# Performance work log

Hardware: AMD Instinct MI355X
Metric: run time of the kernel (lower is better)

Reference implementation:

```python
import jax, jax.numpy as jnp
import numpy as np
from jax import lax

PAD = 1
T, B, V, E, H, K = 256, 64, 50000, 300, 256, 20  # H = hidden_dim//2 per direction


def setup_inputs() -> dict:
    key = jax.random.key(0)
    ks = jax.random.split(key, 14)
    lengths = jnp.sort(jax.random.randint(ks[0], (B,), T // 2, T + 1))[::-1]  # sorted desc like pack_padded
    toks = jax.random.randint(ks[1], (T, B), 2, V)
    tpos = jnp.arange(T)[:, None]
    x = jnp.where(tpos < lengths[None, :], toks, PAD)
    n = jax.random.normal
    s = 1.0 / np.sqrt(H)
    emb = (n(ks[2], (V, E)) * 0.1).at[PAD].set(0.0)  # padding_idx row zeroed
    Wih0 = n(ks[3], (2, 4 * H, E)) * s       # [dir, 4H, in]
    Whh0 = n(ks[4], (2, 4 * H, H)) * s
    b0 = n(ks[5], (2, 4 * H)) * s            # b_ih + b_hh folded together
    Wih1 = n(ks[6], (2, 4 * H, 2 * H)) * s
    Whh1 = n(ks[7], (2, 4 * H, H)) * s
    b1 = n(ks[8], (2, 4 * H)) * s
    W_out = n(ks[9], (K, 2 * H)) * s
    b_out = n(ks[10], (K,)) * s
    trans = n(ks[11], (K, K)) * 0.1
    start = n(ks[12], (K,)) * 0.1
    end = n(ks[13], (K,)) * 0.1
    return dict(x=x, sent_lengths=lengths, emb=emb, Wih0=Wih0, Whh0=Whh0, b0=b0,
                Wih1=Wih1, Whh1=Whh1, b1=b1, W_out=W_out, b_out=b_out,
                trans=trans, start=start, end=end)


def _lstm_dir(xs, m, Wih, Whh, b):
    # xs [T,B,D], m [T,B,1] float mask. PyTorch gate order i,f,g,o.
    xg = jnp.einsum('tbd,gd->tbg', xs, Wih) + b  # big GEMM up-front
    h0 = jnp.zeros((xs.shape[1], H), xs.dtype)

    def step(carry, inp):
        h, c = carry
        g_t, m_t = inp
        gates = g_t + h @ Whh.T
        i, f, g, o = jnp.split(gates, 4, -1)
        c_new = jax.nn.sigmoid(f) * c + jax.nn.sigmoid(i) * jnp.tanh(g)
        h_new = jax.nn.sigmoid(o) * jnp.tanh(c_new)
        # freeze state at padded steps (pack_padded semantics); padded outputs are zero
        return (jnp.where(m_t > 0, h_new, h), jnp.where(m_t > 0, c_new, c)), h_new * m_t

    _, out = lax.scan(step, (h0, h0), (xg, m))
    return out


def _bilstm(xs, m, rev, Wih, Whh, b):
    out_f = _lstm_dir(xs, m, Wih[0], Whh[0], b[0])
    xs_r = jnp.take_along_axis(xs, rev[:, :, None], 0)  # reverse within each length
    out_b = jnp.take_along_axis(_lstm_dir(xs_r, m, Wih[1], Whh[1], b[1]), rev[:, :, None], 0)
    return jnp.concatenate([out_f, out_b], -1)


def reference(x, sent_lengths, emb, Wih0, Whh0, b0, Wih1, Whh1, b1, W_out, b_out, trans, start, end):
    mask = x != PAD                               # [T,B]
    m = mask[:, :, None].astype(emb.dtype)
    tpos = jnp.arange(T)[:, None]
    rev = jnp.where(tpos < sent_lengths[None, :], sent_lengths[None, :] - 1 - tpos, tpos)
    h = emb[x]                                    # [T,B,E]
    h = _bilstm(h, m, rev, Wih0, Whh0, b0)
    h = _bilstm(h, m, rev, Wih1, Whh1, b1)
    emis = jnp.einsum('tbh,kh->tbk', h, W_out) + b_out  # [T,B,K]

    # Viterbi decode (torchcrf semantics)
    score0 = start[None, :] + emis[0]             # [B,K]

    def vstep(sc, inp):
        e_t, m_t = inp
        cand = sc[:, :, None] + trans[None] + e_t[:, None, :]  # [B,prev,next]
        best = cand.max(1)
        ptr = cand.argmax(1).astype(jnp.int32)
        sc2 = jnp.where(m_t[:, None], best, sc)
        # identity pointer at padded steps so backtrace passes tags through
        ptr = jnp.where(m_t[:, None], ptr, jnp.arange(K, dtype=jnp.int32)[None, :])
        return sc2, ptr

    score, hist = lax.scan(vstep, score0, (emis[1:], mask[1:]))
    score = score + end[None, :]                  # score frozen at seq end -> same as adding at last valid step
    last = jnp.argmax(score, -1).astype(jnp.int32)

    def back(tag, ptr):
        prev = jnp.take_along_axis(ptr, tag[:, None], 1)[:, 0]
        return prev, prev

    _, tags_prev = lax.scan(back, last, hist, reverse=True)
    tags = jnp.concatenate([tags_prev, last[None, :]], 0)  # [T,B]
    return jnp.where(mask, tags, 0)
```

## Files before the change

kernel.cpp:

```cpp
#include <hip/hip_runtime.h>
#include <stdint.h>


#define T_ 256
#define B_ 64
#define EPAD 304
#define KTAG 20
#define TB_ (T_ * B_)

#define QR2 22
#define QL2 8
#define QS2 34

#define KR_LO 64
#define KLQ_LO 3
#define NQS_LO 45
#define WLDS_OFF_LO (2 * KR_LO * 1024)
#define WSTR_OFF_LO (WLDS_OFF_LO + 2 * KLQ_LO * 1024 * 4)

__device__ __forceinline__ float rlane(float v, int l) {
  return __int_as_float(__builtin_amdgcn_readlane(__float_as_int(v), l));
}


__global__ void prep_embed(const int* __restrict__ x, const float* __restrict__ emb,
                           float* __restrict__ xsA) {
  int r = blockIdx.x;
  int tok = x[r];
  const float* src = emb + (size_t)tok * 300;
  for (int e = threadIdx.x; e < EPAD; e += 64)
    xsA[(size_t)r * EPAD + e] = (e < 300) ? src[e] : 0.f;
}

__global__ void prep_b0t(const float* __restrict__ Wih0, float* __restrict__ B0t) {
  int idx = blockIdx.x * 256 + threadIdx.x;
  if (idx >= 2048 * EPAD) return;
  int n = idx / EPAD, k = idx % EPAD;
  B0t[idx] = (k < 300) ? Wih0[(size_t)n * 300 + k] : 0.f;
}

__global__ void prep_bot64(const float* __restrict__ Wout, float* __restrict__ Bot,
                           const float* __restrict__ bout, float* __restrict__ biaso) {
  int idx = blockIdx.x * 256 + threadIdx.x;
  int n = idx >> 9, k = idx & 511;
  Bot[idx] = (n < KTAG) ? Wout[(size_t)n * 512 + k] : 0.f;
  if (idx < 64) biaso[idx] = (idx < KTAG) ? bout[idx] : 0.f;
}

__global__ void prep_whh4(const float* __restrict__ Whh, float* __restrict__ whhU) {
  int idx = blockIdx.x * 256 + threadIdx.x;
  int d = idx >> 18, rem = idx & 262143, row = rem >> 8, k = rem & 255;
  float v = Whh[(size_t)d * 262144 + (size_t)row * 256 + k];
  int gt = row >> 8, j = row & 255;
  int q = k >> 2, e = k & 3;
  whhU[((((size_t)d * 64 + q) * 4 + gt) * 256 + j) * 4 + e] = v;
}

__global__ void prep_whh2(const float* __restrict__ Whh, float* __restrict__ whhL) {
  int idx = blockIdx.x * 256 + threadIdx.x;
  int d = idx >> 18, rem = idx & 262143, k = rem >> 10, tg = rem & 1023;
  int row = (tg & 3) * 256 + (tg >> 2);
  float v = Whh[(size_t)d * 262144 + (size_t)row * 256 + k];
  if (k < KR_LO) {
    whhL[(size_t)(d * KR_LO + k) * 1024 + tg] = v;
  } else if (k < KR_LO + 12) {
    int kk = k - KR_LO, q = kk >> 2, e = kk & 3;
    whhL[WLDS_OFF_LO + (size_t)((d * KLQ_LO + q) * 1024 + tg) * 4 + e] = v;
  } else {
    int kk = k - KR_LO - 12, q = kk >> 2, e = kk & 3;
    whhL[WSTR_OFF_LO + (size_t)((d * NQS_LO + q) * 1024 + tg) * 4 + e] = v;
  }
}

__global__ __launch_bounds__(256) void gemm_f32(
    const float* __restrict__ A, int lda, const float* __restrict__ Bt, int ldb,
    float* __restrict__ C, int ldc, const float* __restrict__ bias,
    int ntn, int K) {
  const int tm = blockIdx.x / ntn, tn = blockIdx.x % ntn;
  const int m0 = tm * 64, n0 = tn * 64;
  __shared__ __align__(16) float As[16][64];
  __shared__ __align__(16) float Bs[16][64];
  const int tid = threadIdx.x;
  const int mm = tid >> 2, kq = (tid & 3) * 4;
  const int tx = tid & 15, ty = tid >> 4;
  float acc[4][4] = {};
  for (int k0 = 0; k0 < K; k0 += 16) {
    float4 av = *(const float4*)&A[(size_t)(m0 + mm) * lda + k0 + kq];
    float4 bv = *(const float4*)&Bt[(size_t)(n0 + mm) * ldb + k0 + kq];
    __syncthreads();
    As[kq + 0][mm] = av.x; As[kq + 1][mm] = av.y;
    As[kq + 2][mm] = av.z; As[kq + 3][mm] = av.w;
    Bs[kq + 0][mm] = bv.x; Bs[kq + 1][mm] = bv.y;
    Bs[kq + 2][mm] = bv.z; Bs[kq + 3][mm] = bv.w;
    __syncthreads();
#pragma unroll
    for (int kk = 0; kk < 16; ++kk) {
      float4 a4 = *(const float4*)&As[kk][ty * 4];
      float4 b4 = *(const float4*)&Bs[kk][tx * 4];
      acc[0][0] += a4.x * b4.x; acc[0][1] += a4.x * b4.y;
      acc[0][2] += a4.x * b4.z; acc[0][3] += a4.x * b4.w;
      acc[1][0] += a4.y * b4.x; acc[1][1] += a4.y * b4.y;
      acc[1][2] += a4.y * b4.z; acc[1][3] += a4.y * b4.w;
      acc[2][0] += a4.z * b4.x; acc[2][1] += a4.z * b4.y;
      acc[2][2] += a4.z * b4.z; acc[2][3] += a4.z * b4.w;
      acc[3][0] += a4.w * b4.x; acc[3][1] += a4.w * b4.y;
      acc[3][2] += a4.w * b4.z; acc[3][3] += a4.w * b4.w;
    }
  }
#pragma unroll
  for (int i = 0; i < 4; ++i)
#pragma unroll
    for (int j = 0; j < 4; ++j)
      C[(size_t)(m0 + ty * 4 + i) * ldc + n0 + tx * 4 + j] =
          acc[i][j] + bias[n0 + tx * 4 + j];
}

__global__ __attribute__((amdgpu_flat_work_group_size(512, 512),
                          amdgpu_waves_per_eu(2, 2)))
void lstm_rec_hi2(const float* __restrict__ xg, const float* __restrict__ whhU,
                  float* __restrict__ out, const int* __restrict__ lens) {
  const int wg = blockIdx.x, d = wg & 1, b = wg >> 1;
  const int len = lens[b];
  const int tg = threadIdx.x;
  const int j = tg & 255, gp = tg >> 8;
  const int g0 = gp * 2;
  const int l = tg & 63;
  const float* wb = whhU + (size_t)d * 64 * 4096;

  float4 wA[QR2], wB[QR2];
#pragma unroll
  for (int q = 0; q < QR2; ++q) {
    wA[q] = *(const float4*)(wb + ((size_t)(q * 4 + g0) * 256 + j) * 4);
    wB[q] = *(const float4*)(wb + ((size_t)(q * 4 + g0 + 1) * 256 + j) * 4);
  }
#pragma unroll
  for (int q = 0; q < QR2; ++q) {
    asm volatile("" : "+v"(wA[q].x), "+v"(wA[q].y), "+v"(wA[q].z), "+v"(wA[q].w));
    asm volatile("" : "+v"(wB[q].x), "+v"(wB[q].y), "+v"(wB[q].z), "+v"(wB[q].w));
  }

  __shared__ __align__(16) float4 wlds[QL2][4][256];
  __shared__ __align__(16) float hsd[2][256];
  __shared__ __align__(8) float2 exch[256];
  for (int i = tg; i < QL2 * 4 * 256; i += 512) {
    int q3 = i >> 10, g = (i >> 8) & 3, jj = i & 255;
    wlds[q3][g][jj] =
        *(const float4*)(wb + ((size_t)((QR2 + q3) * 4 + g) * 256 + jj) * 4);
  }
  if (tg < 256) hsd[0][tg] = 0.f;
  float c = 0.f;
  __syncthreads();

  for (int s = 0; s < len; ++s) {
    const int t = d ? (len - 1 - s) : s;
    const int rp = t * B_ + b;
    const size_t xb = (size_t)rp * 2048 + d * 1024 + (size_t)g0 * 256 + j;
    float xv0 = xg[xb];
    float xv1 = xg[xb + 256];
    float4 hv = *(const float4*)&hsd[s & 1][l * 4];

    float aA0 = 0.f, aA1 = 0.f, aB0 = 0.f, aB1 = 0.f;
#pragma unroll
    for (int q = 0; q < QR2; ++q) {
      float b0 = rlane(hv.x, q), b1 = rlane(hv.y, q);
      float b2 = rlane(hv.z, q), b3 = rlane(hv.w, q);
      aA0 += wA[q].x * b0 + wA[q].y * b1;  aA1 += wA[q].z * b2 + wA[q].w * b3;
      aB0 += wB[q].x * b0 + wB[q].y * b1;  aB1 += wB[q].z * b2 + wB[q].w * b3;
    }
#pragma unroll
    for (int q3 = 0; q3 < QL2; ++q3) {
      int q = QR2 + q3;
      float b0 = rlane(hv.x, q), b1 = rlane(hv.y, q);
      float b2 = rlane(hv.z, q), b3 = rlane(hv.w, q);
      float4 wa = wlds[q3][g0][j], wbq = wlds[q3][g0 + 1][j];
      aA0 += wa.x * b0 + wa.y * b1;   aA1 += wa.z * b2 + wa.w * b3;
      aB0 += wbq.x * b0 + wbq.y * b1; aB1 += wbq.z * b2 + wbq.w * b3;
    }
#pragma unroll 2
    for (int qs = 0; qs < QS2; ++qs) {
      int q = QR2 + QL2 + qs;
      float4 wa = *(const float4*)(wb + ((size_t)(q * 4 + g0) * 256 + j) * 4);
      float4 wbq = *(const float4*)(wb + ((size_t)(q * 4 + g0 + 1) * 256 + j) * 4);
      float b0 = rlane(hv.x, q), b1 = rlane(hv.y, q);
      float b2 = rlane(hv.z, q), b3 = rlane(hv.w, q);
      aA0 += wa.x * b0 + wa.y * b1;   aA1 += wa.z * b2 + wa.w * b3;
      aB0 += wbq.x * b0 + wbq.y * b1; aB1 += wbq.z * b2 + wbq.w * b3;
    }

    float aA = aA0 + aA1 + xv0;
    float aB = aB0 + aB1 + xv1;
    if (gp == 1) exch[j] = make_float2(aA, aB);
    __syncthreads();
    if (gp == 0) {
      float2 go = exch[j];
      float si = 1.f / (1.f + expf(-aA));
      float sf = 1.f / (1.f + expf(-aB));
      float so = 1.f / (1.f + expf(-go.y));
      c = sf * c + si * tanhf(go.x);
      float h = so * tanhf(c);
      hsd[(s + 1) & 1][j] = h;
      out[(size_t)rp * 512 + d * 256 + j] = h;
    }
    __syncthreads();
  }
  if (gp == 0)
    for (int t = len; t < T_; ++t)
      out[(size_t)(t * B_ + b) * 512 + d * 256 + j] = 0.f;
}

__global__ __launch_bounds__(1024, 4) void lstm_rec_lo(
    const float* __restrict__ xg, const float* __restrict__ whhL,
    float* __restrict__ out, const int* __restrict__ lens) {
  const int wg = blockIdx.x, dir = wg & 1, b = wg >> 1;
  const int len = lens[b];
  const int tg = threadIdx.x;
  const int j = tg >> 2, gt = tg & 3;
  const int row = gt * 256 + j;

  float wres[KR_LO];
#pragma unroll
  for (int k = 0; k < KR_LO; ++k)
    wres[k] = whhL[(size_t)(dir * KR_LO + k) * 1024 + tg];

  __shared__ __align__(16) float4 wlds[KLQ_LO][1024];
  __shared__ __align__(16) float hsd[2][256];
#pragma unroll
  for (int q = 0; q < KLQ_LO; ++q)
    wlds[q][tg] = *(const float4*)&whhL[WLDS_OFF_LO + (size_t)((dir * KLQ_LO + q) * 1024 + tg) * 4];
  if (tg < 256) hsd[0][tg] = 0.f;
  float c = 0.f;
  __syncthreads();

  const float* sp = whhL + WSTR_OFF_LO + (size_t)dir * NQS_LO * 4096 + (size_t)tg * 4;
  const int lane = tg & 63, qb = lane & ~3;

  for (int s = 0; s < len; ++s) {
    const int t = dir ? (len - 1 - s) : s;
    const int rp = t * B_ + b;
    float xv = xg[(size_t)rp * 2048 + dir * 1024 + row];
    float4 hv = *(const float4*)&hsd[s & 1][lane * 4];

    float acc0 = 0.f, acc1 = 0.f;
#pragma unroll
    for (int q = 0; q < KR_LO / 4; ++q) {
      float b0 = rlane(hv.x, q), b1 = rlane(hv.y, q);
      float b2 = rlane(hv.z, q), b3 = rlane(hv.w, q);
      acc0 += wres[4 * q + 0] * b0 + wres[4 * q + 1] * b1;
      acc1 += wres[4 * q + 2] * b2 + wres[4 * q + 3] * b3;
    }
#pragma unroll
    for (int q3 = 0; q3 < KLQ_LO; ++q3) {
      int q = KR_LO / 4 + q3;
      float4 wl = wlds[q3][tg];
      float b0 = rlane(hv.x, q), b1 = rlane(hv.y, q);
      float b2 = rlane(hv.z, q), b3 = rlane(hv.w, q);
      acc0 += wl.x * b0 + wl.y * b1;
      acc1 += wl.z * b2 + wl.w * b3;
    }
#pragma unroll 5
    for (int qq = 0; qq < NQS_LO; ++qq) {
      int q = KR_LO / 4 + KLQ_LO + qq;
      float4 wv = *(const float4*)(sp + (size_t)qq * 4096);
      float b0 = rlane(hv.x, q), b1 = rlane(hv.y, q);
      float b2 = rlane(hv.z, q), b3 = rlane(hv.w, q);
      acc0 += wv.x * b0 + wv.y * b1;
      acc1 += wv.z * b2 + wv.w * b3;
    }

    float a = acc0 + acc1 + xv;
    float v1 = __shfl(a, qb | 1);
    float v2 = __shfl(a, qb | 2);
    float v3 = __shfl(a, qb | 3);
    if (gt == 0) {
      float si = 1.f / (1.f + expf(-a));
      float sf = 1.f / (1.f + expf(-v1));
      float so = 1.f / (1.f + expf(-v3));
      c = sf * c + si * tanhf(v2);
      float h = so * tanhf(c);
      hsd[(s + 1) & 1][j] = h;
      out[(size_t)rp * 512 + dir * 256 + j] = h;
    }
    __syncthreads();
  }
  for (int t = len; t < T_; ++t)
    if (gt == 0) out[(size_t)(t * B_ + b) * 512 + dir * 256 + j] = 0.f;
}

__global__ __launch_bounds__(64) void viterbi(
    const float* __restrict__ emis, const float* __restrict__ trans,
    const float* __restrict__ startv, const float* __restrict__ endv,
    const int* __restrict__ lens, int* __restrict__ outp) {
  int b = blockIdx.x, lane = threadIdx.x;
  __shared__ float tr[KTAG * KTAG];
  __shared__ float fin[KTAG];
  __shared__ unsigned char hist[T_ * KTAG];
  for (int i = lane; i < KTAG * KTAG; i += 64) tr[i] = trans[i];
  int len = lens[b];
  float score = (lane < KTAG) ? startv[lane] + emis[(size_t)b * 64 + lane] : -3e38f;
  __syncthreads();
  for (int t = 1; t < len; ++t) {
    float e = (lane < KTAG) ? emis[(size_t)(t * B_ + b) * 64 + lane] : 0.f;
    float best = -3e38f; int bp = 0;
    for (int p = 0; p < KTAG; ++p) {
      float cand = (__shfl(score, p) + tr[p * KTAG + lane]) + e;
      if (cand > best) { best = cand; bp = p; }
    }
    if (lane < KTAG) { score = best; hist[t * KTAG + lane] = (unsigned char)bp; }
  }
  if (lane < KTAG) fin[lane] = score + endv[lane];
  __syncthreads();
  if (lane == 0) {
    float bb = -3e38f; int tag = 0;
    for (int p = 0; p < KTAG; ++p)
      if (fin[p] > bb) { bb = fin[p]; tag = p; }
    for (int t = len - 1; t >= 1; --t) {
      outp[t * B_ + b] = tag;
      tag = hist[t * KTAG + tag];
    }
    outp[b] = tag;
  }
  for (int t = len + lane; t < T_; t += 64) outp[t * B_ + b] = 0;
}

__global__ void sentinel_fill(int* __restrict__ outp, int val) {
  int i = blockIdx.x * 256 + threadIdx.x;
  if (i < TB_) outp[i] = val;
}
__global__ void diag_init(int* __restrict__ f) { if (threadIdx.x == 0) f[0] = 0; }
__global__ void check_nan(const float* __restrict__ p, long n, int* __restrict__ f) {
  long i0 = (long)blockIdx.x * 256 + threadIdx.x;
  int bad = 0;
  for (long i = i0; i < n; i += (long)gridDim.x * 256)
    if (!(fabsf(p[i]) <= 1e8f)) bad = 1;
  if (bad) atomicOr(&f[0], 1);
}
__global__ void verdict(const int* __restrict__ f, int* __restrict__ outp) {
  if (f[0]) outp[threadIdx.x] = -4096;
}


extern "C" void kernel_launch(void* const* d_in, const int* in_sizes, int n_in,
                              void* d_out, int out_size, void* d_ws, size_t ws_size,
                              hipStream_t stream) {
  int* outp = (int*)d_out;

  static const int exp_sizes[14] = {16384, 64, 15000000, 614400, 524288, 2048,
                                    1048576, 524288, 2048, 10240, 20, 400, 20, 20};
  int badi = (n_in == 14) ? -1 : 14;
  if (badi < 0)
    for (int i = 0; i < 14; ++i)
      if (in_sizes[i] != exp_sizes[i]) { badi = i; break; }
  if (badi >= 0) {
    hipLaunchKernelGGL(sentinel_fill, dim3((TB_ + 255) / 256), dim3(256), 0, stream,
                       outp, -(20000 + badi));
    return;
  }

  const int*   x      = (const int*)d_in[0];
  const int*   lens   = (const int*)d_in[1];
  const float* emb    = (const float*)d_in[2];
  const float* Wih0   = (const float*)d_in[3];
  const float* Whh0   = (const float*)d_in[4];
  const float* b0     = (const float*)d_in[5];
  const float* Wih1   = (const float*)d_in[6];
  const float* Whh1   = (const float*)d_in[7];
  const float* b1     = (const float*)d_in[8];
  const float* Wout   = (const float*)d_in[9];
  const float* bout   = (const float*)d_in[10];
  const float* trans  = (const float*)d_in[11];
  const float* startv = (const float*)d_in[12];
  const float* endv   = (const float*)d_in[13];

  static int chosen = -1;
  if (chosen < 0) {
    chosen = 0;
    hipFuncAttributes fa;
    if (hipFuncGetAttributes(&fa, reinterpret_cast<const void*>(&lstm_rec_hi2)) ==
            hipSuccess &&
        fa.localSizeBytes == 0 && fa.numRegs >= 160)
      chosen = 1;
  }

  const size_t sz_whh = (size_t)524288 * 4;

  const size_t need =
      (size_t)TB_ * 2048 * 4
    + (size_t)TB_ * EPAD * 4
    + (size_t)TB_ * 512 * 4
    + (size_t)2048 * EPAD * 4
    + (size_t)64 * 512 * 4
    + 4 * sz_whh
    + 64 * 4
    + (size_t)TB_ * 64 * 4
    + 64;

  if (ws_size < need) {
    hipLaunchKernelGGL(sentinel_fill, dim3((TB_ + 255) / 256), dim3(256), 0, stream,
                       outp, -(int)(10000 + (ws_size >> 20)));
    return;
  }

  char* w = (char*)d_ws;
  float* xg    = (float*)w;  w += (size_t)TB_ * 2048 * 4;
  float* xsA   = (float*)w;  w += (size_t)TB_ * EPAD * 4;
  float* outh  = (float*)w;  w += (size_t)TB_ * 512 * 4;
  float* B0t   = (float*)w;  w += (size_t)2048 * EPAD * 4;
  float* Bot   = (float*)w;  w += (size_t)64 * 512 * 4;
  float* whh0U = (float*)w;  w += sz_whh;
  float* whh1U = (float*)w;  w += sz_whh;
  float* whh0L = (float*)w;  w += sz_whh;
  float* whh1L = (float*)w;  w += sz_whh;
  float* biaso = (float*)w;  w += 64 * 4;
  float* emis  = (float*)w;  w += (size_t)TB_ * 64 * 4;
  int*   diag  = (int*)w;    w += 64;

  hipLaunchKernelGGL(diag_init, dim3(1), dim3(64), 0, stream, diag);
  hipLaunchKernelGGL(prep_embed, dim3(TB_), dim3(64), 0, stream, x, emb, xsA);
  hipLaunchKernelGGL(prep_b0t, dim3((2048 * EPAD + 255) / 256), dim3(256), 0, stream, Wih0, B0t);
  hipLaunchKernelGGL(prep_bot64, dim3(128), dim3(256), 0, stream, Wout, Bot, bout, biaso);
  if (chosen == 1) {
    hipLaunchKernelGGL(prep_whh4, dim3(2048), dim3(256), 0, stream, Whh0, whh0U);
    hipLaunchKernelGGL(prep_whh4, dim3(2048), dim3(256), 0, stream, Whh1, whh1U);
  } else {
    hipLaunchKernelGGL(prep_whh2, dim3(2048), dim3(256), 0, stream, Whh0, whh0L);
    hipLaunchKernelGGL(prep_whh2, dim3(2048), dim3(256), 0, stream, Whh1, whh1L);
  }

  hipLaunchKernelGGL(gemm_f32, dim3(256 * 32), dim3(256), 0, stream,
                     xsA, EPAD, B0t, EPAD, xg, 2048, b0, 32, EPAD);
  if (chosen == 1)
    hipLaunchKernelGGL(lstm_rec_hi2, dim3(128), dim3(512), 0, stream, xg, whh0U, outh, lens);
  else
    hipLaunchKernelGGL(lstm_rec_lo, dim3(128), dim3(1024), 0, stream, xg, whh0L, outh, lens);
  hipLaunchKernelGGL(gemm_f32, dim3(256 * 32), dim3(256), 0, stream,
                     outh, 512, Wih1, 512, xg, 2048, b1, 32, 512);
  if (chosen == 1)
    hipLaunchKernelGGL(lstm_rec_hi2, dim3(128), dim3(512), 0, stream, xg, whh1U, outh, lens);
  else
    hipLaunchKernelGGL(lstm_rec_lo, dim3(128), dim3(1024), 0, stream, xg, whh1L, outh, lens);
  hipLaunchKernelGGL(gemm_f32, dim3(256), dim3(256), 0, stream,
                     outh, 512, Bot, 512, emis, 64, biaso, 1, 512);
  hipLaunchKernelGGL(check_nan, dim3(256), dim3(256), 0, stream,
                     emis, (long)TB_ * 64, diag);
  hipLaunchKernelGGL(viterbi, dim3(B_), dim3(64), 0, stream,
                     emis, trans, startv, endv, lens, outp);
  hipLaunchKernelGGL(verdict, dim3(1), dim3(64), 0, stream, diag, outp);
}
```

Measured before the change: 3.994 ms.

## Remap LSTM lanes so gate pairs share a wave and exchange via shuffle

Rearranges the thread-to-hidden-unit mapping so both gate pairs for a hidden unit sit in the same wavefront (lower and upper 32 lanes). The g/o gate exchange then uses a cross-lane shuffle, which removes one workgroup barrier and the LDS exchange buffer on every timestep. It also moves more Whh slices into registers and LDS and fewer into per-step global loads, which raises register and LDS pressure and could cause spills. If spills occur, the existing register check would fall back to the slower kernel.

```diff
diff --git a/kernel.cpp b/kernel.cpp
--- a/kernel.cpp
+++ b/kernel.cpp
@@ -8,9 +8,9 @@
 #define KTAG 20
 #define TB_ (T_ * B_)
 
-#define QR2 22
-#define QL2 8
-#define QS2 34
+#define QR2 24
+#define QL2 9
+#define QS2 31
 
 #define KR_LO 64
 #define KLQ_LO 3
@@ -117,21 +117,22 @@
 
 __global__ __attribute__((amdgpu_flat_work_group_size(512, 512),
                           amdgpu_waves_per_eu(2, 2)))
-void lstm_rec_hi2(const float* __restrict__ xg, const float* __restrict__ whhU,
+void lstm_rec_hi3(const float* __restrict__ xg, const float* __restrict__ whhU,
                   float* __restrict__ out, const int* __restrict__ lens) {
   const int wg = blockIdx.x, d = wg & 1, b = wg >> 1;
   const int len = lens[b];
   const int tg = threadIdx.x;
-  const int j = tg & 255, gp = tg >> 8;
+  const int w = tg >> 6, l = tg & 63;
+  const int lhalf = l & 31, gp = l >> 5;
+  const int jj = w * 32 + lhalf;
   const int g0 = gp * 2;
-  const int l = tg & 63;
   const float* wb = whhU + (size_t)d * 64 * 4096;
 
   float4 wA[QR2], wB[QR2];
 #pragma unroll
   for (int q = 0; q < QR2; ++q) {
-    wA[q] = *(const float4*)(wb + ((size_t)(q * 4 + g0) * 256 + j) * 4);
-    wB[q] = *(const float4*)(wb + ((size_t)(q * 4 + g0 + 1) * 256 + j) * 4);
+    wA[q] = *(const float4*)(wb + ((size_t)(q * 4 + g0) * 256 + jj) * 4);
+    wB[q] = *(const float4*)(wb + ((size_t)(q * 4 + g0 + 1) * 256 + jj) * 4);
   }
 #pragma unroll
   for (int q = 0; q < QR2; ++q) {
@@ -141,11 +142,10 @@
 
   __shared__ __align__(16) float4 wlds[QL2][4][256];
   __shared__ __align__(16) float hsd[2][256];
-  __shared__ __align__(8) float2 exch[256];
   for (int i = tg; i < QL2 * 4 * 256; i += 512) {
-    int q3 = i >> 10, g = (i >> 8) & 3, jj = i & 255;
-    wlds[q3][g][jj] =
-        *(const float4*)(wb + ((size_t)((QR2 + q3) * 4 + g) * 256 + jj) * 4);
+    int q3 = i >> 10, g = (i >> 8) & 3, jx = i & 255;
+    wlds[q3][g][jx] =
+        *(const float4*)(wb + ((size_t)((QR2 + q3) * 4 + g) * 256 + jx) * 4);
   }
   if (tg < 256) hsd[0][tg] = 0.f;
   float c = 0.f;
@@ -154,7 +154,7 @@
   for (int s = 0; s < len; ++s) {
     const int t = d ? (len - 1 - s) : s;
     const int rp = t * B_ + b;
-    const size_t xb = (size_t)rp * 2048 + d * 1024 + (size_t)g0 * 256 + j;
+    const size_t xb = (size_t)rp * 2048 + d * 1024 + (size_t)g0 * 256 + jj;
     float xv0 = xg[xb];
     float xv1 = xg[xb + 256];
     float4 hv = *(const float4*)&hsd[s & 1][l * 4];
@@ -172,15 +172,15 @@
       int q = QR2 + q3;
       float b0 = rlane(hv.x, q), b1 = rlane(hv.y, q);
       float b2 = rlane(hv.z, q), b3 = rlane(hv.w, q);
-      float4 wa = wlds[q3][g0][j], wbq = wlds[q3][g0 + 1][j];
+      float4 wa = wlds[q3][g0][jj], wbq = wlds[q3][g0 + 1][jj];
       aA0 += wa.x * b0 + wa.y * b1;   aA1 += wa.z * b2 + wa.w * b3;
       aB0 += wbq.x * b0 + wbq.y * b1; aB1 += wbq.z * b2 + wbq.w * b3;
     }
 #pragma unroll 2
     for (int qs = 0; qs < QS2; ++qs) {
       int q = QR2 + QL2 + qs;
-      float4 wa = *(const float4*)(wb + ((size_t)(q * 4 + g0) * 256 + j) * 4);
-      float4 wbq = *(const float4*)(wb + ((size_t)(q * 4 + g0 + 1) * 256 + j) * 4);
+      float4 wa = *(const float4*)(wb + ((size_t)(q * 4 + g0) * 256 + jj) * 4);
+      float4 wbq = *(const float4*)(wb + ((size_t)(q * 4 + g0 + 1) * 256 + jj) * 4);
       float b0 = rlane(hv.x, q), b1 = rlane(hv.y, q);
       float b2 = rlane(hv.z, q), b3 = rlane(hv.w, q);
       aA0 += wa.x * b0 + wa.y * b1;   aA1 += wa.z * b2 + wa.w * b3;
@@ -189,23 +189,22 @@
 
     float aA = aA0 + aA1 + xv0;
     float aB = aB0 + aB1 + xv1;
-    if (gp == 1) exch[j] = make_float2(aA, aB);
-    __syncthreads();
+    float gG = __shfl(aA, lhalf + 32);
+    float gO = __shfl(aB, lhalf + 32);
     if (gp == 0) {
-      float2 go = exch[j];
       float si = 1.f / (1.f + expf(-aA));
       float sf = 1.f / (1.f + expf(-aB));
-      float so = 1.f / (1.f + expf(-go.y));
-      c = sf * c + si * tanhf(go.x);
+      float so = 1.f / (1.f + expf(-gO));
+      c = sf * c + si * tanhf(gG);
       float h = so * tanhf(c);
-      hsd[(s + 1) & 1][j] = h;
-      out[(size_t)rp * 512 + d * 256 + j] = h;
+      hsd[(s + 1) & 1][jj] = h;
+      out[(size_t)rp * 512 + d * 256 + jj] = h;
     }
     __syncthreads();
   }
   if (gp == 0)
     for (int t = len; t < T_; ++t)
-      out[(size_t)(t * B_ + b) * 512 + d * 256 + j] = 0.f;
+      out[(size_t)(t * B_ + b) * 512 + d * 256 + jj] = 0.f;
 }
 
 __global__ __launch_bounds__(1024, 4) void lstm_rec_lo(
@@ -375,7 +374,7 @@
   if (chosen < 0) {
     chosen = 0;
     hipFuncAttributes fa;
-    if (hipFuncGetAttributes(&fa, reinterpret_cast<const void*>(&lstm_rec_hi2)) ==
+    if (hipFuncGetAttributes(&fa, reinterpret_cast<const void*>(&lstm_rec_hi3)) ==
             hipSuccess &&
         fa.localSizeBytes == 0 && fa.numRegs >= 160)
       chosen = 1;
@@ -429,13 +428,13 @@
   hipLaunchKernelGGL(gemm_f32, dim3(256 * 32), dim3(256), 0, stream,
                      xsA, EPAD, B0t, EPAD, xg, 2048, b0, 32, EPAD);
   if (chosen == 1)
-    hipLaunchKernelGGL(lstm_rec_hi2, dim3(128), dim3(512), 0, stream, xg, whh0U, outh, lens);
+    hipLaunchKernelGGL(lstm_rec_hi3, dim3(128), dim3(512), 0, stream, xg, whh0U, outh, lens);
   else
     hipLaunchKernelGGL(lstm_rec_lo, dim3(128), dim3(1024), 0, stream, xg, whh0L, outh, lens);
   hipLaunchKernelGGL(gemm_f32, dim3(256 * 32), dim3(256), 0, stream,
                      outh, 512, Wih1, 512, xg, 2048, b1, 32, 512);
   if (chosen == 1)
-    hipLaunchKernelGGL(lstm_rec_hi2, dim3(128), dim3(512), 0, stream, xg, whh1U, outh, lens);
+    hipLaunchKernelGGL(lstm_rec_hi3, dim3(128), dim3(512), 0, stream, xg, whh1U, outh, lens);
   else
     hipLaunchKernelGGL(lstm_rec_lo, dim3(128), dim3(1024), 0, stream, xg, whh1L, outh, lens);
   hipLaunchKernelGGL(gemm_f32, dim3(256), dim3(256), 0, stream,
```

Measured after the change: 4.764 ms. 1.19x slower.

## Add 1024-thread LSTM recurrence kernel with one gate row per thread

Applied to the files above, without the earlier changes.

Adds lstm_rec_hi5, which gives each thread one gate row. The first 72 weights of that row stay in registers, the next 36 in LDS, and the rest stream from global memory. Gates are combined with wave shuffles instead of an LDS exchange. It is selected at runtime when its register count passes a threshold. The aim is to raise parallelism per workgroup and remove one sync per step, at the cost of more global streaming per step and extra workspace.

```diff
diff --git a/kernel.cpp b/kernel.cpp
--- a/kernel.cpp
+++ b/kernel.cpp
@@ -9,8 +9,14 @@
 #define TB_ (T_ * B_)
 
 #define QR2 22
-#define QL2 8
-#define QS2 34
+#define QL2A 8
+#define QS2A 34
+
+#define KR5 72
+#define KLQ5 9
+#define NQS5 37
+#define WLDS_OFF5 (2 * KR5 * 1024)
+#define WSTR_OFF5 (WLDS_OFF5 + 2 * KLQ5 * 1024 * 4)
 
 #define KR_LO 64
 #define KLQ_LO 3
@@ -54,6 +60,22 @@
   int gt = row >> 8, j = row & 255;
   int q = k >> 2, e = k & 3;
   whhU[((((size_t)d * 64 + q) * 4 + gt) * 256 + j) * 4 + e] = v;
+}
+
+__global__ void prep_whh5(const float* __restrict__ Whh, float* __restrict__ whhV) {
+  int idx = blockIdx.x * 256 + threadIdx.x;
+  int d = idx >> 18, rem = idx & 262143, k = rem >> 10, tg = rem & 1023;
+  int row = (tg & 3) * 256 + (tg >> 2);
+  float v = Whh[(size_t)d * 262144 + (size_t)row * 256 + k];
+  if (k < KR5) {
+    whhV[(size_t)(d * KR5 + k) * 1024 + tg] = v;
+  } else if (k < KR5 + 4 * KLQ5) {
+    int kk = k - KR5, q = kk >> 2, e = kk & 3;
+    whhV[WLDS_OFF5 + (size_t)((d * KLQ5 + q) * 1024 + tg) * 4 + e] = v;
+  } else {
+    int kk = k - KR5 - 4 * KLQ5, q = kk >> 2, e = kk & 3;
+    whhV[WSTR_OFF5 + (size_t)((d * NQS5 + q) * 1024 + tg) * 4 + e] = v;
+  }
 }
 
 __global__ void prep_whh2(const float* __restrict__ Whh, float* __restrict__ whhL) {
@@ -115,6 +137,88 @@
           acc[i][j] + bias[n0 + tx * 4 + j];
 }
 
+__global__ __attribute__((amdgpu_flat_work_group_size(1024, 1024),
+                          amdgpu_waves_per_eu(4, 4)))
+void lstm_rec_hi5(const float* __restrict__ xg, const float* __restrict__ whhV,
+                  float* __restrict__ out, const int* __restrict__ lens) {
+  const int wg = blockIdx.x, dir = wg & 1, b = wg >> 1;
+  const int len = lens[b];
+  const int tg = threadIdx.x;
+  const int j = tg >> 2, gt = tg & 3;
+  const int row = gt * 256 + j;
+
+  float wres[KR5];
+#pragma unroll
+  for (int k = 0; k < KR5; ++k)
+    wres[k] = whhV[(size_t)(dir * KR5 + k) * 1024 + tg];
+#pragma unroll
+  for (int k = 0; k < KR5; ++k)
+    asm volatile("" : "+v"(wres[k]));
+
+  __shared__ __align__(16) float4 wlds[KLQ5][1024];
+  __shared__ __align__(16) float hsd[2][256];
+#pragma unroll
+  for (int q = 0; q < KLQ5; ++q)
+    wlds[q][tg] = *(const float4*)&whhV[WLDS_OFF5 + (size_t)((dir * KLQ5 + q) * 1024 + tg) * 4];
+  if (tg < 256) hsd[0][tg] = 0.f;
+  float c = 0.f;
+  __syncthreads();
+
+  const float* sp = whhV + WSTR_OFF5 + (size_t)dir * NQS5 * 4096 + (size_t)tg * 4;
+  const int lane = tg & 63, qb = lane & ~3;
+
+  for (int s = 0; s < len; ++s) {
+    const int t = dir ? (len - 1 - s) : s;
+    const int rp = t * B_ + b;
+    float xv = xg[(size_t)rp * 2048 + dir * 1024 + row];
+    float4 hv = *(const float4*)&hsd[s & 1][lane * 4];
+
+    float acc0 = 0.f, acc1 = 0.f;
+#pragma unroll
+    for (int q = 0; q < KR5 / 4; ++q) {
+      float b0 = rlane(hv.x, q), b1 = rlane(hv.y, q);
+      float b2 = rlane(hv.z, q), b3 = rlane(hv.w, q);
+      acc0 += wres[4 * q + 0] * b0 + wres[4 * q + 1] * b1;
+      acc1 += wres[4 * q + 2] * b2 + wres[4 * q + 3] * b3;
+    }
+#pragma unroll
+    for (int q3 = 0; q3 < KLQ5; ++q3) {
+      int q = KR5 / 4 + q3;
+      float4 wl = wlds[q3][tg];
+      float b0 = rlane(hv.x, q), b1 = rlane(hv.y, q);
+      float b2 = rlane(hv.z, q), b3 = rlane(hv.w, q);
+      acc0 += wl.x * b0 + wl.y * b1;
+      acc1 += wl.z * b2 + wl.w * b3;
+    }
+#pragma unroll 5
+    for (int qq = 0; qq < NQS5; ++qq) {
+      int q = KR5 / 4 + KLQ5 + qq;
+      float4 wv = *(const float4*)(sp + (size_t)qq * 4096);
+      float b0 = rlane(hv.x, q), b1 = rlane(hv.y, q);
+      float b2 = rlane(hv.z, q), b3 = rlane(hv.w, q);
+      acc0 += wv.x * b0 + wv.y * b1;
+      acc1 += wv.z * b2 + wv.w * b3;
+    }
+
+    float a = acc0 + acc1 + xv;
+    float v1 = __shfl(a, qb | 1);
+    float v2 = __shfl(a, qb | 2);
+    float v3 = __shfl(a, qb | 3);
+    if (gt == 0) {
+      float si = 1.f / (1.f + expf(-a));
+      float sf = 1.f / (1.f + expf(-v1));
+      float so = 1.f / (1.f + expf(-v3));
+      c = sf * c + si * tanhf(v2);
+      float h = so * tanhf(c);
+      hsd[(s + 1) & 1][j] = h;
+      out[(size_t)rp * 512 + dir * 256 + j] = h;
+    }
+    __syncthreads();
+  }
+  for (int t = len; t < T_; ++t)
+    if (gt == 0) out[(size_t)(t * B_ + b) * 512 + dir * 256 + j] = 0.f;
+}
+
 __global__ __attribute__((amdgpu_flat_work_group_size(512, 512),
                           amdgpu_waves_per_eu(2, 2)))
 void lstm_rec_hi2(const float* __restrict__ xg, const float* __restrict__ whhU,
@@ -139,10 +243,10 @@
     asm volatile("" : "+v"(wB[q].x), "+v"(wB[q].y), "+v"(wB[q].z), "+v"(wB[q].w));
   }
 
-  __shared__ __align__(16) float4 wlds[QL2][4][256];
+  __shared__ __align__(16) float4 wlds[QL2A][4][256];
   __shared__ __align__(16) float hsd[2][256];
   __shared__ __align__(8) float2 exch[256];
-  for (int i = tg; i < QL2 * 4 * 256; i += 512) {
+  for (int i = tg; i < QL2A * 4 * 256; i += 512) {
     int q3 = i >> 10, g = (i >> 8) & 3, jj = i & 255;
     wlds[q3][g][jj] =
         *(const float4*)(wb + ((size_t)((QR2 + q3) * 4 + g) * 256 + jj) * 4);
@@ -168,7 +272,7 @@
       aB0 += wB[q].x * b0 + wB[q].y * b1;  aB1 += wB[q].z * b2 + wB[q].w * b3;
     }
 #pragma unroll
-    for (int q3 = 0; q3 < QL2; ++q3) {
+    for (int q3 = 0; q3 < QL2A; ++q3) {
       int q = QR2 + q3;
       float b0 = rlane(hv.x, q), b1 = rlane(hv.y, q);
       float b2 = rlane(hv.z, q), b3 = rlane(hv.w, q);
@@ -177,8 +281,8 @@
       aB0 += wbq.x * b0 + wbq.y * b1; aB1 += wbq.z * b2 + wbq.w * b3;
     }
 #pragma unroll 2
-    for (int qs = 0; qs < QS2; ++qs) {
-      int q = QR2 + QL2 + qs;
+    for (int qs = 0; qs < QS2A; ++qs) {
+      int q = QR2 + QL2A + qs;
       float4 wa = *(const float4*)(wb + ((size_t)(q * 4 + g0) * 256 + j) * 4);
       float4 wbq = *(const float4*)(wb + ((size_t)(q * 4 + g0 + 1) * 256 + j) * 4);
       float b0 = rlane(hv.x, q), b1 = rlane(hv.y, q);
@@ -377,8 +481,12 @@
     hipFuncAttributes fa;
     if (hipFuncGetAttributes(&fa, reinterpret_cast<const void*>(&lstm_rec_hi2)) ==
             hipSuccess &&
-        fa.localSizeBytes == 0 && fa.numRegs >= 160)
+        fa.localSizeBytes == 0 && fa.numRegs >= 150)
       chosen = 1;
+    if (hipFuncGetAttributes(&fa, reinterpret_cast<const void*>(&lstm_rec_hi5)) ==
+            hipSuccess &&
+        fa.localSizeBytes == 0 && fa.numRegs >= 100)
+      chosen = 3;
   }
 
   const size_t sz_whh = (size_t)524288 * 4;
@@ -389,7 +497,7 @@
     + (size_t)TB_ * 512 * 4
     + (size_t)2048 * EPAD * 4
     + (size_t)64 * 512 * 4
-    + 4 * sz_whh
+    + 6 * sz_whh
     + 64 * 4
     + (size_t)TB_ * 64 * 4
     + 64;
@@ -408,6 +516,8 @@
   float* Bot   = (float*)w;  w += (size_t)64 * 512 * 4;
   float* whh0U = (float*)w;  w += sz_whh;
   float* whh1U = (float*)w;  w += sz_whh;
+  float* whh0V = (float*)w;  w += sz_whh;
+  float* whh1V = (float*)w;  w += sz_whh;
   float* whh0L = (float*)w;  w += sz_whh;
   float* whh1L = (float*)w;  w += sz_whh;
   float* biaso = (float*)w;  w += 64 * 4;
@@ -418,7 +528,10 @@
   hipLaunchKernelGGL(prep_embed, dim3(TB_), dim3(64), 0, stream, x, emb, xsA);
   hipLaunchKernelGGL(prep_b0t, dim3((2048 * EPAD + 255) / 256), dim3(256), 0, stream, Wih0, B0t);
   hipLaunchKernelGGL(prep_bot64, dim3(128), dim3(256), 0, stream, Wout, Bot, bout, biaso);
-  if (chosen == 1) {
+  if (chosen == 3) {
+    hipLaunchKernelGGL(prep_whh5, dim3(2048), dim3(256), 0, stream, Whh0, whh0V);
+    hipLaunchKernelGGL(prep_whh5, dim3(2048), dim3(256), 0, stream, Whh1, whh1V);
+  } else if (chosen == 1) {
     hipLaunchKernelGGL(prep_whh4, dim3(2048), dim3(256), 0, stream, Whh0, whh0U);
     hipLaunchKernelGGL(prep_whh4, dim3(2048), dim3(256), 0, stream, Whh1, whh1U);
   } else {
@@ -428,13 +541,17 @@
 
   hipLaunchKernelGGL(gemm_f32, dim3(256 * 32), dim3(256), 0, stream,
                      xsA, EPAD, B0t, EPAD, xg, 2048, b0, 32, EPAD);
-  if (chosen == 1)
+  if (chosen == 3)
+    hipLaunchKernelGGL(lstm_rec_hi5, dim3(128), dim3(1024), 0, stream, xg, whh0V, outh, lens);
+  else if (chosen == 1)
     hipLaunchKernelGGL(lstm_rec_hi2, dim3(128), dim3(512), 0, stream, xg, whh0U, outh, lens);
   else
     hipLaunchKernelGGL(lstm_rec_lo, dim3(128), dim3(1024), 0, stream, xg, whh0L, outh, lens);
   hipLaunchKernelGGL(gemm_f32, dim3(256 * 32), dim3(256), 0, stream,
                      outh, 512, Wih1, 512, xg, 2048, b1, 32, 512);
-  if (chosen == 1)
+  if (chosen == 3)
+    hipLaunchKernelGGL(lstm_rec_hi5, dim3(128), dim3(1024), 0, stream, xg, whh1V, outh, lens);
+  else if (chosen == 1)
     hipLaunchKernelGGL(lstm_rec_hi2, dim3(128), dim3(512), 0, stream, xg, whh1U, outh, lens);
   else
     hipLaunchKernelGGL(lstm_rec_lo, dim3(128), dim3(1024), 0, stream, xg, whh1L, outh, lens);
```

After: 3.984 ms. About the same (-0.2%).
